# Performance work log

Hardware: AMD Instinct MI355X
Metric: run time of the kernel (lower is better)

The kernel has to match this reference:

```python
import jax, jax.numpy as jnp
import numpy as np

N = 50000
E = 800000
F_IN = 128


def _gat(h, src, dst, W, a_src, a_dst, bias, heads, out_ch, concat):
    n = h.shape[0]
    z = (h @ W.T).reshape(n, heads, out_ch)              # [N,H,C]
    alpha_s = jnp.sum(z * a_src, axis=-1)                # [N,H]
    alpha_d = jnp.sum(z * a_dst, axis=-1)                # [N,H]
    logits = jax.nn.leaky_relu(alpha_s[src] + alpha_d[dst], 0.2)  # [Etot,H]
    m = jax.ops.segment_max(logits, dst, num_segments=n)
    ex = jnp.exp(logits - m[dst])
    denom = jax.ops.segment_sum(ex, dst, num_segments=n)
    w = ex / (denom[dst] + 1e-16)                        # [Etot,H]
    agg = jax.ops.segment_sum(w[:, :, None] * z[src], dst, num_segments=n)  # [N,H,C]
    if concat:
        out = agg.reshape(n, heads * out_ch)
    else:
        out = agg.mean(axis=1)
    return out + bias


def setup_inputs() -> dict:
    key = jax.random.key(0)
    ks = jax.random.split(key, 16)
    s = lambda *sh: 1.0 / np.sqrt(sh[-1])
    inp = {
        "x": jax.random.normal(ks[0], (N, F_IN), jnp.float32),
        "edge_index": jax.random.randint(ks[1], (2, E), 0, N, jnp.int64),
        # GraphConv(no_node_features=128 -> 128, aggr='add')
        "W_rel": jax.random.normal(ks[2], (128, F_IN), jnp.float32) * s(128, F_IN),
        "b_rel": jnp.zeros((128,), jnp.float32),
        "W_root": jax.random.normal(ks[3], (128, F_IN), jnp.float32) * s(128, F_IN),
        # GATConv(128 -> 8, heads=8, concat) => 64
        "W1": jax.random.normal(ks[4], (64, 128), jnp.float32) * s(64, 128),
        "a1_src": jax.random.normal(ks[5], (8, 8), jnp.float32) * 0.35,
        "a1_dst": jax.random.normal(ks[6], (8, 8), jnp.float32) * 0.35,
        "b1": jnp.zeros((64,), jnp.float32),
        # GATConv(64 -> 64, heads=1, concat=False)
        "W2": jax.random.normal(ks[7], (64, 64), jnp.float32) * s(64, 64),
        "a2_src": jax.random.normal(ks[8], (1, 64), jnp.float32) * 0.125,
        "a2_dst": jax.random.normal(ks[9], (1, 64), jnp.float32) * 0.125,
        "b2": jnp.zeros((64,), jnp.float32),
        "Wr": jax.random.normal(ks[10], (1, 64), jnp.float32) * s(1, 64),
        "br": jnp.zeros((1,), jnp.float32),
    }
    return inp


def reference(x, edge_index, W_rel, b_rel, W_root, W1, a1_src, a1_dst, b1,
              W2, a2_src, a2_dst, b2, Wr, br):
    src, dst = edge_index[0], edge_index[1]
    # GraphConv, aggr='add': W_rel @ sum_{j in N(i)} x_j + b + W_root @ x_i
    nbr = jax.ops.segment_sum(x[src], dst, num_segments=N)
    h = nbr @ W_rel.T + b_rel + x @ W_root.T
    h = jax.nn.elu(h)
    # GATConv adds self-loops by default
    loop = jnp.arange(N, dtype=edge_index.dtype)
    src2 = jnp.concatenate([src, loop])
    dst2 = jnp.concatenate([dst, loop])
    h = _gat(h, src2, dst2, W1, a1_src, a1_dst, b1, heads=8, out_ch=8, concat=True)
    h = jax.nn.elu(h)
    h = _gat(h, src2, dst2, W2, a2_src, a2_dst, b2, heads=1, out_ch=64, concat=False)
    # final 'mean' aggregation over all nodes (single graph)
    g = jnp.mean(h, axis=0, keepdims=True)               # [1,64]
    return g @ Wr.T + br                                  # [1,1]
```

## Files before the change

### kernel.cpp

```cpp
#include <hip/hip_runtime.h>
#include <hip/hip_bf16.h>
#include <math.h>

#define N_NODES 50000
#define N_EDGES 800000
#define F_IN 128
#define NBUCK 391
#define EPB 4096
#define NBB 196

typedef __attribute__((ext_vector_type(8))) short bf16x8;
typedef __attribute__((ext_vector_type(4))) float f32x4;
typedef __attribute__((ext_vector_type(2))) float f32x2;
typedef unsigned long long ull;

__device__ __forceinline__ float elu_f(float x)   { return x > 0.f ? x : expm1f(x); }
__device__ __forceinline__ float lrelu_f(float x) { return x > 0.f ? x : 0.2f * x; }
__device__ __forceinline__ int   clampN(int v)    { return v < 0 ? 0 : (v >= N_NODES ? N_NODES - 1 : v); }
__device__ __forceinline__ float bits2f(unsigned int u) { union { unsigned int u; float f; } x; x.u = u; return x.f; }
__device__ __forceinline__ float bf2f(unsigned short s) { return bits2f(((unsigned int)s) << 16); }
__device__ __forceinline__ unsigned short f2bfbits(float f) {
    __hip_bfloat16 b = __float2bfloat16(f);
    return __builtin_bit_cast(unsigned short, b);
}
__device__ __forceinline__ unsigned int pack2(float lo, float hi) {
    return ((unsigned int)f2bfbits(hi) << 16) | f2bfbits(lo);
}

#define CAST_X_IDS (N_NODES * 32)
#define CAST_IDS (CAST_X_IDS + 32768 + 8192 + 4096)
#define CASTB ((CAST_IDS + 255) / 256)
__global__ __launch_bounds__(256) void k_prep(const int* __restrict__ dst,
                                              const float* __restrict__ x,
                                              const float* __restrict__ W_rel,
                                              const float* __restrict__ W_root,
                                              const float* __restrict__ W1,
                                              const float* __restrict__ W2,
                                              int* __restrict__ part,
                                              __hip_bfloat16* __restrict__ Abuf,
                                              unsigned int* __restrict__ x8,
                                              __hip_bfloat16* __restrict__ Wc,
                                              __hip_bfloat16* __restrict__ W1b,
                                              __hip_bfloat16* __restrict__ W2b,
                                              float* __restrict__ red) {
    __shared__ int hist[NBUCK];
    int tid = threadIdx.x;
    if (blockIdx.x < NBB) {
        for (int j = tid; j < NBUCK; j += 256) hist[j] = 0;
        __syncthreads();
        int base = blockIdx.x * EPB;
        #pragma unroll
        for (int t = 0; t < EPB / 256; ++t) {
            int e = base + t * 256 + tid;
            if (e < N_EDGES) atomicAdd(&hist[clampN(dst[e]) >> 7], 1);
        }
        __syncthreads();
        for (int j = tid; j < NBUCK; j += 256)
            part[(size_t)blockIdx.x * NBUCK + j] = hist[j];
    } else {
        if (blockIdx.x == NBB) red[tid] = 0.f;
        int id = (blockIdx.x - NBB) * 256 + tid;
        if (id < CAST_X_IDS) {
            int i = id >> 5, c4 = (id & 31) * 4;
            float4 v = *(const float4*)&x[(size_t)i * 128 + c4];
            ull p = (ull)f2bfbits(v.x) | ((ull)f2bfbits(v.y) << 16)
                  | ((ull)f2bfbits(v.z) << 32) | ((ull)f2bfbits(v.w) << 48);
            *(ull*)&Abuf[(size_t)i * 256 + 128 + c4] = p;
            int t = __builtin_amdgcn_cvt_pk_fp8_f32(v.x, v.y, 0, false);
            t = __builtin_amdgcn_cvt_pk_fp8_f32(v.z, v.w, t, true);
            x8[(size_t)i * 32 + (id & 31)] = (unsigned int)t;
        } else if (id < CAST_IDS) {
            int j = id - CAST_X_IDS;
            if (j < 32768) {
                int cc = j >> 8, k = j & 255;
                float v = (k < 128) ? W_rel[cc * 128 + k] : W_root[cc * 128 + (k - 128)];
                Wc[j] = __float2bfloat16(v);
            } else if (j < 32768 + 8192) {
                W1b[j - 32768] = __float2bfloat16(W1[j - 32768]);
            } else {
                W2b[j - 32768 - 8192] = __float2bfloat16(W2[j - 32768 - 8192]);
            }
        }
    }
}

__global__ __launch_bounds__(512) void k_bscan(const int* __restrict__ part,
                                               int* __restrict__ boff,
                                               int* __restrict__ bcur) {
    __shared__ int wsum[8];
    __shared__ int wbase[8];
    int tid = threadIdx.x;
    int lane = tid & 63, wid = tid >> 6;
    int v = 0;
    if (tid < NBUCK) {
        for (int b = 0; b < NBB; ++b) v += part[(size_t)b * NBUCK + tid];
    }
    int x = v;
    #pragma unroll
    for (int d = 1; d < 64; d <<= 1) {
        int t = __shfl_up(x, d, 64);
        if (lane >= d) x += t;
    }
    if (lane == 63) wsum[wid] = x;
    __syncthreads();
    if (tid == 0) {
        int b = 0;
        #pragma unroll
        for (int w = 0; w < 8; ++w) { wbase[w] = b; b += wsum[w]; }
    }
    __syncthreads();
    if (tid < NBUCK) {
        int e = wbase[wid] + x - v;
        boff[tid] = e;
        bcur[tid] = e;
    }
    if (tid == 0) boff[NBUCK] = N_EDGES;
}

__global__ __launch_bounds__(256) void k_bscatter(const int* __restrict__ src,
                                                  const int* __restrict__ dst,
                                                  int* __restrict__ bcur,
                                                  unsigned int* __restrict__ ebuf) {
    __shared__ int hist[NBUCK];
    __shared__ int hbase[NBUCK];
    int tid = threadIdx.x;
    for (int j = tid; j < NBUCK; j += 256) hist[j] = 0;
    __syncthreads();
    int base = blockIdx.x * EPB;
    unsigned int myP[EPB / 256]; int myB[EPB / 256], myR[EPB / 256];
    #pragma unroll
    for (int t = 0; t < EPB / 256; ++t) {
        int e = base + t * 256 + tid;
        if (e < N_EDGES) {
            int d = clampN(dst[e]);
            int s = clampN(src[e]);
            myP[t] = ((unsigned int)s << 7) | (unsigned int)(d & 127);
            myB[t] = d >> 7;
            myR[t] = atomicAdd(&hist[d >> 7], 1);
        } else myB[t] = -1;
    }
    __syncthreads();
    for (int j = tid; j < NBUCK; j += 256)
        if (hist[j]) hbase[j] = atomicAdd(&bcur[j], hist[j]);
    __syncthreads();
    #pragma unroll
    for (int t = 0; t < EPB / 256; ++t) {
        if (myB[t] >= 0) ebuf[hbase[myB[t]] + myR[t]] = myP[t];
    }
}

__global__ __launch_bounds__(256) void k_bfinal(const unsigned int* __restrict__ ebuf,
                                                const int* __restrict__ boff,
                                                int* __restrict__ offsets,
                                                int* __restrict__ csr) {
    __shared__ int cnt[128];
    __shared__ int cur[128];
    __shared__ int ws[4];
    int b = blockIdx.x;
    int tid = threadIdx.x;
    int node0 = b << 7;
    int k0 = boff[b], k1 = boff[b + 1];
    if (tid < 128) cnt[tid] = 0;
    __syncthreads();
    for (int k = k0 + tid; k < k1; k += 256)
        atomicAdd(&cnt[ebuf[k] & 127u], 1);
    __syncthreads();
    int lane = tid & 63;
    int v = (tid < 128) ? cnt[tid] : 0;
    int x = v;
    #pragma unroll
    for (int d = 1; d < 64; d <<= 1) {
        int t = __shfl_up(x, d, 64);
        if (lane >= d) x += t;
    }
    if (lane == 63) ws[tid >> 6] = x;
    __syncthreads();
    if (tid < 128) {
        int add = (tid >> 6) ? ws[0] : 0;
        int excl = k0 + add + x - v;
        cur[tid] = excl;
        int node = node0 + tid;
        if (node < N_NODES) offsets[node] = excl;
    }
    if (b == NBUCK - 1 && tid == 0) offsets[N_NODES] = N_EDGES;
    __syncthreads();
    for (int k = k0 + tid; k < k1; k += 256) {
        unsigned int e = ebuf[k];
        int r = atomicAdd(&cur[e & 127u], 1);
        csr[r] = (int)(e >> 7);
    }
}

__global__ __launch_bounds__(256) void k_gather(const unsigned int* __restrict__ x8,
                                                const int* __restrict__ offsets,
                                                const int* __restrict__ csr,
                                                ull* __restrict__ outNbr) {
    int i = blockIdx.x * 8 + (threadIdx.x >> 5);
    int l = threadIdx.x & 31;
    int k0 = offsets[i], k1 = offsets[i + 1];
    float a0 = 0.f, a1 = 0.f, a2 = 0.f, a3 = 0.f;
    for (int kb = k0; kb < k1; kb += 8) {
        int s[8]; int vm[8];
        #pragma unroll
        for (int j = 0; j < 8; ++j) {
            int kk = kb + j;
            vm[j] = kk < k1;
            s[j] = csr[vm[j] ? kk : k1 - 1];
        }
        unsigned int u[8];
        #pragma unroll
        for (int j = 0; j < 8; ++j) u[j] = x8[(size_t)s[j] * 32 + l];
        #pragma unroll
        for (int j = 0; j < 8; ++j) {
            if (vm[j]) {
                f32x2 lo = __builtin_amdgcn_cvt_pk_f32_fp8(u[j], false);
                f32x2 hi = __builtin_amdgcn_cvt_pk_f32_fp8(u[j], true);
                a0 += lo.x; a1 += lo.y; a2 += hi.x; a3 += hi.y;
            }
        }
    }
    outNbr[(size_t)i * 64 + l] = (ull)pack2(a0, a1) | ((ull)pack2(a2, a3) << 32);
}

__global__ __launch_bounds__(256) void k_gemm12(const __hip_bfloat16* __restrict__ A,
                                                const __hip_bfloat16* __restrict__ Wc,
                                                const float* __restrict__ bias,
                                                const __hip_bfloat16* __restrict__ W1b,
                                                const float* __restrict__ a_src,
                                                const float* __restrict__ a_dst,
                                                float* __restrict__ as_o,
                                                float* __restrict__ ad_o,
                                                unsigned int* __restrict__ z8) {
    __shared__ __align__(16) short smem[64 * 136];
    short (*sA)[40] = (short(*)[40])smem;
    short (*sW)[40] = (short(*)[40])(smem + 64 * 40);
    int tid = threadIdx.x;
    int lane = tid & 63, wave = tid >> 6;
    int quad = lane >> 4, l16 = lane & 15;
    int node0 = blockIdx.x * 64;
    int srow = tid >> 2, schk = (tid & 3) * 8;
    int ga = node0 + srow; if (ga >= N_NODES) ga = N_NODES - 1;
    const short* Ap = (const short*)A + (size_t)ga * 256 + schk;
    const short* Wp = (const short*)Wc;
    f32x4 acc[8];
    #pragma unroll
    for (int t = 0; t < 8; ++t) acc[t] = (f32x4){0.f, 0.f, 0.f, 0.f};
    for (int k0 = 0; k0 < 256; k0 += 32) {
        *(bf16x8*)&sA[srow][schk] = *(const bf16x8*)(Ap + k0);
        #pragma unroll
        for (int it = 0; it < 2; ++it) {
            int wrow = srow + it * 64;
            *(bf16x8*)&sW[wrow][schk] = *(const bf16x8*)(Wp + (size_t)wrow * 256 + k0 + schk);
        }
        __syncthreads();
        bf16x8 a = *(const bf16x8*)&sA[wave * 16 + l16][quad * 8];
        #pragma unroll
        for (int nt = 0; nt < 8; ++nt) {
            bf16x8 b = *(const bf16x8*)&sW[nt * 16 + l16][quad * 8];
            acc[nt] = __builtin_amdgcn_mfma_f32_16x16x32_bf16(a, b, acc[nt], 0, 0, 0);
        }
        __syncthreads();
    }
    #pragma unroll
    for (int nt = 0; nt < 8; ++nt) {
        int col = nt * 16 + l16;
        float bv = bias[col];
        #pragma unroll
        for (int r = 0; r < 4; ++r) {
            int row = wave * 16 + quad * 4 + r;
            smem[row * 136 + col] = (short)f2bfbits(elu_f(acc[nt][r] + bv));
        }
    }
    __syncthreads();
    f32x4 acc2[4];
    #pragma unroll
    for (int t = 0; t < 4; ++t) acc2[t] = (f32x4){0.f, 0.f, 0.f, 0.f};
    const short* W1p = (const short*)W1b;
    #pragma unroll
    for (int k0 = 0; k0 < 128; k0 += 32) {
        bf16x8 a = *(const bf16x8*)&smem[(wave * 16 + l16) * 136 + k0 + quad * 8];
        #pragma unroll
        for (int nt = 0; nt < 4; ++nt) {
            bf16x8 b = *(const bf16x8*)(W1p + (size_t)(nt * 16 + l16) * 128 + k0 + quad * 8);
            acc2[nt] = __builtin_amdgcn_mfma_f32_16x16x32_bf16(a, b, acc2[nt], 0, 0, 0);
        }
    }
    __syncthreads();
    #pragma unroll
    for (int nt = 0; nt < 4; ++nt) {
        int col = nt * 16 + l16;
        #pragma unroll
        for (int r = 0; r < 4; ++r) {
            int row = wave * 16 + quad * 4 + r;
            smem[row * 72 + col] = (short)f2bfbits(acc2[nt][r]);
        }
    }
    __syncthreads();
    int row = tid >> 2, chunk = tid & 3;
    int gi = node0 + row;
    float v[16];
    bf16x8 c0 = *(const bf16x8*)&smem[row * 72 + chunk * 16];
    bf16x8 c1 = *(const bf16x8*)&smem[row * 72 + chunk * 16 + 8];
    #pragma unroll
    for (int j = 0; j < 8; ++j) {
        v[j]     = bf2f((unsigned short)c0[j]);
        v[8 + j] = bf2f((unsigned short)c1[j]);
    }
    float ps0 = 0.f, pd0 = 0.f, ps1 = 0.f, pd1 = 0.f;
    #pragma unroll
    for (int j = 0; j < 8; ++j) {
        ps0 += v[j] * a_src[chunk * 16 + j];
        pd0 += v[j] * a_dst[chunk * 16 + j];
        ps1 += v[8 + j] * a_src[chunk * 16 + 8 + j];
        pd1 += v[8 + j] * a_dst[chunk * 16 + 8 + j];
    }
    if (gi < N_NODES) {
        as_o[(size_t)gi * 8 + 2 * chunk]     = ps0;
        as_o[(size_t)gi * 8 + 2 * chunk + 1] = ps1;
        ad_o[(size_t)gi * 8 + 2 * chunk]     = pd0;
        ad_o[(size_t)gi * 8 + 2 * chunk + 1] = pd1;
        #pragma unroll
        for (int wi = 0; wi < 4; ++wi) {
            int t = __builtin_amdgcn_cvt_pk_fp8_f32(v[4 * wi], v[4 * wi + 1], 0, false);
            t = __builtin_amdgcn_cvt_pk_fp8_f32(v[4 * wi + 2], v[4 * wi + 3], t, true);
            z8[(size_t)gi * 16 + chunk * 4 + wi] = (unsigned int)t;
        }
    }
}

__global__ __launch_bounds__(256) void k_gat1z2(const unsigned int* __restrict__ z8,
                                                const float* __restrict__ as1,
                                                const float* __restrict__ ad1,
                                                const float* __restrict__ b1,
                                                const int* __restrict__ offsets,
                                                const int* __restrict__ csr,
                                                const __hip_bfloat16* __restrict__ W2b,
                                                const float* __restrict__ a2s,
                                                const float* __restrict__ a2d,
                                                float* __restrict__ as2,
                                                float* __restrict__ ad2,
                                                unsigned int* __restrict__ z2e8) {
    __shared__ __align__(16) short sH2[16 * 72];
    __shared__ __align__(16) short sZ2[16 * 72];
    int iloc = threadIdx.x >> 4;
    int i = blockIdx.x * 16 + iloc;
    int l = threadIdx.x & 15;
    int hd = l >> 1;
    int wh = l & 7, slot = l >> 3;
    int k0 = offsets[i], k1 = offsets[i + 1];
    float ad_h = ad1[(size_t)i * 8 + hd];
    float adw  = ad1[(size_t)i * 8 + wh];
    float e_self = __expf(lrelu_f(as1[(size_t)i * 8 + hd] + ad_h));
    unsigned int uz = z8[(size_t)i * 16 + l];
    f32x2 zlo = __builtin_amdgcn_cvt_pk_f32_fp8(uz, false);
    f32x2 zhi = __builtin_amdgcn_cvt_pk_f32_fp8(uz, true);
    float acc0 = e_self * zlo.x, acc1 = e_self * zlo.y;
    float acc2 = e_self * zhi.x, acc3 = e_self * zhi.y;
    float denp = 0.f;
    for (int kb = k0; kb < k1; kb += 8) {
        int sr[4]; float er[4];
        #pragma unroll
        for (int m = 0; m < 4; ++m) {
            int kk = kb + 2 * m + slot;
            bool v = kk < k1;
            int s = csr[v ? kk : k1 - 1];
            sr[m] = s;
            er[m] = v ? __expf(lrelu_f(as1[(size_t)s * 8 + wh] + adw)) : 0.f;
            denp += er[m];
        }
        int sj[8]; float ej[8]; unsigned int u[8];
        #pragma unroll
        for (int m = 0; m < 4; ++m) {
            #pragma unroll
            for (int sb = 0; sb < 2; ++sb) {
                sj[2 * m + sb] = __shfl(sr[m], sb * 8 + hd, 16);
                ej[2 * m + sb] = __shfl(er[m], sb * 8 + hd, 16);
            }
        }
        #pragma unroll
        for (int j = 0; j < 8; ++j) u[j] = z8[(size_t)sj[j] * 16 + l];
        #pragma unroll
        for (int j = 0; j < 8; ++j) {
            f32x2 alo = __builtin_amdgcn_cvt_pk_f32_fp8(u[j], false);
            f32x2 ahi = __builtin_amdgcn_cvt_pk_f32_fp8(u[j], true);
            acc0 += ej[j] * alo.x; acc1 += ej[j] * alo.y;
            acc2 += ej[j] * ahi.x; acc3 += ej[j] * ahi.y;
        }
    }
    denp += __shfl_xor(denp, 8, 16);
    float den = __shfl(denp, hd, 16) + e_self;
    float inv = 1.f / den;
    float r0 = elu_f(acc0 * inv + b1[4 * l + 0]);
    float r1 = elu_f(acc1 * inv + b1[4 * l + 1]);
    float r2 = elu_f(acc2 * inv + b1[4 * l + 2]);
    float r3 = elu_f(acc3 * inv + b1[4 * l + 3]);
    *(ull*)&sH2[iloc * 72 + 4 * l] = (ull)pack2(r0, r1) | ((ull)pack2(r2, r3) << 32);
    __syncthreads();
    int lane = threadIdx.x & 63, wave = threadIdx.x >> 6;
    int quad = lane >> 4, l16 = lane & 15;
    f32x4 accz = (f32x4){0.f, 0.f, 0.f, 0.f};
    const short* W2p = (const short*)W2b;
    #pragma unroll
    for (int kk0 = 0; kk0 < 64; kk0 += 32) {
        bf16x8 a = *(const bf16x8*)&sH2[l16 * 72 + kk0 + quad * 8];
        bf16x8 b = *(const bf16x8*)(W2p + (size_t)(wave * 16 + l16) * 64 + kk0 + quad * 8);
        accz = __builtin_amdgcn_mfma_f32_16x16x32_bf16(a, b, accz, 0, 0, 0);
    }
    #pragma unroll
    for (int r = 0; r < 4; ++r)
        sZ2[(quad * 4 + r) * 72 + wave * 16 + l16] = (short)f2bfbits(accz[r]);
    __syncthreads();
    ull pz = *(const ull*)&sZ2[iloc * 72 + 4 * l];
    float v0 = bf2f((unsigned short)(pz & 0xffff));
    float v1 = bf2f((unsigned short)((pz >> 16) & 0xffff));
    float v2 = bf2f((unsigned short)((pz >> 32) & 0xffff));
    float v3 = bf2f((unsigned short)(pz >> 48));
    float ps = v0 * a2s[4 * l + 0] + v1 * a2s[4 * l + 1] + v2 * a2s[4 * l + 2] + v3 * a2s[4 * l + 3];
    float pd = v0 * a2d[4 * l + 0] + v1 * a2d[4 * l + 1] + v2 * a2d[4 * l + 2] + v3 * a2d[4 * l + 3];
    #pragma unroll
    for (int d = 8; d >= 1; d >>= 1) {
        ps += __shfl_xor(ps, d, 16);
        pd += __shfl_xor(pd, d, 16);
    }
    if (l == 0) { as2[i] = ps; ad2[i] = pd; }
    int t = __builtin_amdgcn_cvt_pk_fp8_f32(v0, v1, 0, false);
    t = __builtin_amdgcn_cvt_pk_fp8_f32(v2, v3, t, true);
    z2e8[(size_t)i * 16 + l] = (unsigned int)t;
}

__global__ __launch_bounds__(256) void k_gat2attn(const unsigned int* __restrict__ z8,
                                                  const float* __restrict__ as2,
                                                  const float* __restrict__ ad2,
                                                  const float* __restrict__ b2,
                                                  const int* __restrict__ offsets,
                                                  const int* __restrict__ csr,
                                                  const float* __restrict__ Wr,
                                                  float* __restrict__ red) {
    int i = blockIdx.x * 16 + (threadIdx.x >> 4);
    int l = threadIdx.x & 15;
    int k0 = offsets[i], k1 = offsets[i + 1];
    float ad = ad2[i];
    float e_self = __expf(lrelu_f(as2[i] + ad));
    unsigned int uz = z8[(size_t)i * 16 + l];
    f32x2 zlo = __builtin_amdgcn_cvt_pk_f32_fp8(uz, false);
    f32x2 zhi = __builtin_amdgcn_cvt_pk_f32_fp8(uz, true);
    float acc0 = e_self * zlo.x, acc1 = e_self * zlo.y;
    float acc2 = e_self * zhi.x, acc3 = e_self * zhi.y;
    float denp = (l == 0) ? e_self : 0.f;
    for (int kb = k0; kb < k1; kb += 16) {
        int kk = kb + l;
        bool v = kk < k1;
        int s = csr[v ? kk : k1 - 1];
        float e = v ? __expf(lrelu_f(as2[s] + ad)) : 0.f;
        denp += e;
        int nv = k1 - kb; if (nv > 16) nv = 16;
        for (int j0 = 0; j0 < nv; j0 += 8) {
            int sj[8]; float ej[8]; unsigned int u[8];
            #pragma unroll
            for (int j = 0; j < 8; ++j) {
                int idx = (j0 + j) & 15;
                sj[j] = __shfl(s, idx, 16);
                ej[j] = __shfl(e, idx, 16);
            }
            #pragma unroll
            for (int j = 0; j < 8; ++j) u[j] = z8[(size_t)sj[j] * 16 + l];
            #pragma unroll
            for (int j = 0; j < 8; ++j) {
                f32x2 alo = __builtin_amdgcn_cvt_pk_f32_fp8(u[j], false);
                f32x2 ahi = __builtin_amdgcn_cvt_pk_f32_fp8(u[j], true);
                acc0 += ej[j] * alo.x; acc1 += ej[j] * alo.y;
                acc2 += ej[j] * ahi.x; acc3 += ej[j] * ahi.y;
            }
        }
    }
    #pragma unroll
    for (int d = 8; d >= 1; d >>= 1) denp += __shfl_xor(denp, d, 16);
    float inv = 1.f / denp;
    float c = (acc0 * inv + b2[4 * l + 0]) * Wr[4 * l + 0]
            + (acc1 * inv + b2[4 * l + 1]) * Wr[4 * l + 1]
            + (acc2 * inv + b2[4 * l + 2]) * Wr[4 * l + 2]
            + (acc3 * inv + b2[4 * l + 3]) * Wr[4 * l + 3];
    #pragma unroll
    for (int d = 8; d >= 1; d >>= 1) c += __shfl_xor(c, d, 64);
    if (l == 0) atomicAdd(&red[blockIdx.x & 255], c);
}

__global__ void k_finalize(const float* __restrict__ red, const float* __restrict__ br,
                           float* __restrict__ out) {
    int t = threadIdx.x;
    float s = red[t] + red[t + 64] + red[t + 128] + red[t + 192];
    #pragma unroll
    for (int d = 32; d >= 1; d >>= 1) s += __shfl_xor(s, d, 64);
    if (t == 0) out[0] = s * (1.0f / N_NODES) + br[0];
}

extern "C" void kernel_launch(void* const* d_in, const int* in_sizes, int n_in,
                              void* d_out, int out_size, void* d_ws, size_t ws_size,
                              hipStream_t stream) {
    const float* x      = (const float*)d_in[0];
    const int*   edges  = (const int*)d_in[1];
    const float* W_rel  = (const float*)d_in[2];
    const float* b_rel  = (const float*)d_in[3];
    const float* W_root = (const float*)d_in[4];
    const float* W1     = (const float*)d_in[5];
    const float* a1s    = (const float*)d_in[6];
    const float* a1d    = (const float*)d_in[7];
    const float* b1     = (const float*)d_in[8];
    const float* W2     = (const float*)d_in[9];
    const float* a2s    = (const float*)d_in[10];
    const float* a2d    = (const float*)d_in[11];
    const float* b2     = (const float*)d_in[12];
    const float* Wr     = (const float*)d_in[13];
    const float* br     = (const float*)d_in[14];
    float* out = (float*)d_out;

    const int* src = edges;
    const int* dst = edges + N_EDGES;

    char* ws = (char*)d_ws;
    size_t p = 0;
    auto alloc = [&](size_t bytes) -> void* {
        void* r = ws + p;
        p = (p + bytes + 255) & ~(size_t)255;
        return r;
    };
    int*   part    = (int*)alloc((size_t)NBB * NBUCK * 4);
    int*   boff    = (int*)alloc((size_t)(NBUCK + 1) * 4);
    int*   bcur    = (int*)alloc((size_t)NBUCK * 4);
    unsigned int* ebuf = (unsigned int*)alloc((size_t)N_EDGES * 4);
    int*   offsets = (int*)alloc((size_t)(N_NODES + 1) * 4);
    int*   csr     = (int*)alloc((size_t)N_EDGES * 4);
    __hip_bfloat16* Abuf = (__hip_bfloat16*)alloc((size_t)N_NODES * 256 * 2);
    unsigned int* x8 = (unsigned int*)alloc((size_t)N_NODES * 32 * 4);
    __hip_bfloat16* Wc   = (__hip_bfloat16*)alloc((size_t)128 * 256 * 2);
    __hip_bfloat16* W1b  = (__hip_bfloat16*)alloc((size_t)64 * 128 * 2);
    __hip_bfloat16* W2b  = (__hip_bfloat16*)alloc((size_t)64 * 64 * 2);
    float* as1 = (float*)alloc((size_t)N_NODES * 8 * 4);
    float* ad1 = (float*)alloc((size_t)N_NODES * 8 * 4);
    float* as2 = (float*)alloc((size_t)N_NODES * 4);
    float* ad2 = (float*)alloc((size_t)N_NODES * 4);
    unsigned int* z1e8 = (unsigned int*)alloc((size_t)N_NODES * 16 * 4);
    unsigned int* z2e8 = (unsigned int*)alloc((size_t)N_NODES * 16 * 4);
    float* red = (float*)alloc(256 * 4);

    const int MB   = (N_NODES + 63) / 64;
    const int NB8  = N_NODES / 8;
    const int NB16 = N_NODES / 16;

    k_prep    <<<NBB + CASTB, 256, 0, stream>>>(dst, x, W_rel, W_root, W1, W2,
                                                part, Abuf, x8, Wc, W1b, W2b, red);
    k_bscan   <<<1, 512, 0, stream>>>(part, boff, bcur);
    k_bscatter<<<NBB, 256, 0, stream>>>(src, dst, bcur, ebuf);
    k_bfinal  <<<NBUCK, 256, 0, stream>>>(ebuf, boff, offsets, csr);
    k_gather  <<<NB8, 256, 0, stream>>>(x8, offsets, csr, (ull*)Abuf);
    k_gemm12  <<<MB, 256, 0, stream>>>(Abuf, Wc, b_rel, W1b, a1s, a1d, as1, ad1, z1e8);
    k_gat1z2  <<<NB16, 256, 0, stream>>>(z1e8, as1, ad1, b1, offsets, csr,
                                         W2b, a2s, a2d, as2, ad2, z2e8);
    k_gat2attn<<<NB16, 256, 0, stream>>>(z2e8, as2, ad2, b2, offsets, csr, Wr, red);
    k_finalize<<<1, 64, 0, stream>>>(red, br, out);
}
```

Before: 241.6 us.

## Sort nodes by degree into a permutation to balance per-wave work in gather kernels

Builds a degree histogram while the CSR is finalized, then adds a k_perm kernel that counting-sorts node ids into degree bins. The gather and both GAT kernels then process nodes in permuted order, so the lanes of a wave handle nodes with similar edge counts and less time is lost to divergent loop trip counts. The cost is an extra kernel launch, the histogram atomics, and an indirection that scatters node-level loads and stores (offsets, as/ad, outputs) away from sequential order. Degrees are capped into the last bin.

```diff
diff --git a/kernel.cpp b/kernel.cpp
--- a/kernel.cpp
+++ b/kernel.cpp
@@ -8,6 +8,7 @@
 #define NBUCK 391
 #define EPB 4096
 #define NBB 196
+#define NDEGB 64
 
 typedef __attribute__((ext_vector_type(8))) short bf16x8;
 typedef __attribute__((ext_vector_type(4))) float f32x4;
@@ -86,10 +87,14 @@
 
 __global__ __launch_bounds__(512) void k_bscan(const int* __restrict__ part,
                                                int* __restrict__ boff,
-                                               int* __restrict__ bcur) {
+                                               int* __restrict__ bcur,
+                                               int* __restrict__ degHist,
+                                               int* __restrict__ gcur) {
     __shared__ int wsum[8];
     __shared__ int wbase[8];
     int tid = threadIdx.x;
+    if (tid < NDEGB) gcur[tid] = 0;
+    if (tid >= NDEGB && tid < 2 * NDEGB) degHist[tid - NDEGB] = 0;
     int lane = tid & 63, wid = tid >> 6;
     int v = 0;
     if (tid < NBUCK) {
@@ -152,19 +157,29 @@
 __global__ __launch_bounds__(256) void k_bfinal(const unsigned int* __restrict__ ebuf,
                                                 const int* __restrict__ boff,
                                                 int* __restrict__ offsets,
-                                                int* __restrict__ csr) {
+                                                int* __restrict__ csr,
+                                                int* __restrict__ degHist) {
     __shared__ int cnt[128];
     __shared__ int cur[128];
     __shared__ int ws[4];
+    __shared__ int dh[NDEGB];
     int b = blockIdx.x;
     int tid = threadIdx.x;
     int node0 = b << 7;
     int k0 = boff[b], k1 = boff[b + 1];
     if (tid < 128) cnt[tid] = 0;
+    if (tid >= 128 && tid < 128 + NDEGB) dh[tid - 128] = 0;
     __syncthreads();
     for (int k = k0 + tid; k < k1; k += 256)
         atomicAdd(&cnt[ebuf[k] & 127u], 1);
     __syncthreads();
+    if (tid < 128) {
+        int node = node0 + tid;
+        if (node < N_NODES) {
+            int dgb = cnt[tid] > (NDEGB - 1) ? (NDEGB - 1) : cnt[tid];
+            atomicAdd(&dh[dgb], 1);
+        }
+    }
     int lane = tid & 63;
     int v = (tid < 128) ? cnt[tid] : 0;
     int x = v;
@@ -184,6 +199,7 @@
     }
     if (b == NBUCK - 1 && tid == 0) offsets[N_NODES] = N_EDGES;
     __syncthreads();
+    if (tid < NDEGB && dh[tid]) atomicAdd(&degHist[tid], dh[tid]);
     for (int k = k0 + tid; k < k1; k += 256) {
         unsigned int e = ebuf[k];
         int r = atomicAdd(&cur[e & 127u], 1);
@@ -191,11 +207,45 @@
     }
 }
 
+__global__ __launch_bounds__(256) void k_perm(const int* __restrict__ offsets,
+                                              const int* __restrict__ degHist,
+                                              int* __restrict__ gcur,
+                                              int* __restrict__ perm) {
+    __shared__ int base[NDEGB];
+    __shared__ int lh[NDEGB];
+    __shared__ int lbase[NDEGB];
+    int tid = threadIdx.x;
+    if (tid < NDEGB) {
+        int v = degHist[tid];
+        int x = v;
+        #pragma unroll
+        for (int d = 1; d < NDEGB; d <<= 1) {
+            int t = __shfl_up(x, d, 64);
+            if (tid >= d) x += t;
+        }
+        base[tid] = x - v;
+        lh[tid] = 0;
+    }
+    __syncthreads();
+    int i = blockIdx.x * 256 + tid;
+    int bin = 0, rank = 0;
+    if (i < N_NODES) {
+        int deg = offsets[i + 1] - offsets[i];
+        bin = deg > (NDEGB - 1) ? (NDEGB - 1) : deg;
+        rank = atomicAdd(&lh[bin], 1);
+    }
+    __syncthreads();
+    if (tid < NDEGB && lh[tid]) lbase[tid] = atomicAdd(&gcur[tid], lh[tid]);
+    __syncthreads();
+    if (i < N_NODES) perm[base[bin] + lbase[bin] + rank] = i;
+}
+
 __global__ __launch_bounds__(256) void k_gather(const unsigned int* __restrict__ x8,
                                                 const int* __restrict__ offsets,
                                                 const int* __restrict__ csr,
+                                                const int* __restrict__ perm,
                                                 ull* __restrict__ outNbr) {
-    int i = blockIdx.x * 8 + (threadIdx.x >> 5);
+    int i = perm[blockIdx.x * 8 + (threadIdx.x >> 5)];
     int l = threadIdx.x & 31;
     int k0 = offsets[i], k1 = offsets[i + 1];
     float a0 = 0.f, a1 = 0.f, a2 = 0.f, a3 = 0.f;
@@ -334,6 +384,7 @@
                                                 const float* __restrict__ b1,
                                                 const int* __restrict__ offsets,
                                                 const int* __restrict__ csr,
+                                                const int* __restrict__ perm,
                                                 const __hip_bfloat16* __restrict__ W2b,
                                                 const float* __restrict__ a2s,
                                                 const float* __restrict__ a2d,
@@ -343,7 +394,7 @@
     __shared__ __align__(16) short sH2[16 * 72];
     __shared__ __align__(16) short sZ2[16 * 72];
     int iloc = threadIdx.x >> 4;
-    int i = blockIdx.x * 16 + iloc;
+    int i = perm[blockIdx.x * 16 + iloc];
     int l = threadIdx.x & 15;
     int hd = l >> 1;
     int wh = l & 7, slot = l >> 3;
@@ -434,9 +485,10 @@
                                                   const float* __restrict__ b2,
                                                   const int* __restrict__ offsets,
                                                   const int* __restrict__ csr,
+                                                  const int* __restrict__ perm,
                                                   const float* __restrict__ Wr,
                                                   float* __restrict__ red) {
-    int i = blockIdx.x * 16 + (threadIdx.x >> 4);
+    int i = perm[blockIdx.x * 16 + (threadIdx.x >> 4)];
     int l = threadIdx.x & 15;
     int k0 = offsets[i], k1 = offsets[i + 1];
     float ad = ad2[i];
@@ -530,6 +582,9 @@
     unsigned int* ebuf = (unsigned int*)alloc((size_t)N_EDGES * 4);
     int*   offsets = (int*)alloc((size_t)(N_NODES + 1) * 4);
     int*   csr     = (int*)alloc((size_t)N_EDGES * 4);
+    int*   degHist = (int*)alloc((size_t)NDEGB * 4);
+    int*   gcur    = (int*)alloc((size_t)NDEGB * 4);
+    int*   perm    = (int*)alloc((size_t)N_NODES * 4);
     __hip_bfloat16* Abuf = (__hip_bfloat16*)alloc((size_t)N_NODES * 256 * 2);
     unsigned int* x8 = (unsigned int*)alloc((size_t)N_NODES * 32 * 4);
     __hip_bfloat16* Wc   = (__hip_bfloat16*)alloc((size_t)128 * 256 * 2);
@@ -546,16 +601,18 @@
     const int MB   = (N_NODES + 63) / 64;
     const int NB8  = N_NODES / 8;
     const int NB16 = N_NODES / 16;
+    const int PB   = (N_NODES + 255) / 256;
 
     k_prep    <<<NBB + CASTB, 256, 0, stream>>>(dst, x, W_rel, W_root, W1, W2,
                                                 part, Abuf, x8, Wc, W1b, W2b, red);
-    k_bscan   <<<1, 512, 0, stream>>>(part, boff, bcur);
+    k_bscan   <<<1, 512, 0, stream>>>(part, boff, bcur, degHist, gcur);
     k_bscatter<<<NBB, 256, 0, stream>>>(src, dst, bcur, ebuf);
-    k_bfinal  <<<NBUCK, 256, 0, stream>>>(ebuf, boff, offsets, csr);
-    k_gather  <<<NB8, 256, 0, stream>>>(x8, offsets, csr, (ull*)Abuf);
+    k_bfinal  <<<NBUCK, 256, 0, stream>>>(ebuf, boff, offsets, csr, degHist);
+    k_perm    <<<PB, 256, 0, stream>>>(offsets, degHist, gcur, perm);
+    k_gather  <<<NB8, 256, 0, stream>>>(x8, offsets, csr, perm, (ull*)Abuf);
     k_gemm12  <<<MB, 256, 0, stream>>>(Abuf, Wc, b_rel, W1b, a1s, a1d, as1, ad1, z1e8);
-    k_gat1z2  <<<NB16, 256, 0, stream>>>(z1e8, as1, ad1, b1, offsets, csr,
+    k_gat1z2  <<<NB16, 256, 0, stream>>>(z1e8, as1, ad1, b1, offsets, csr, perm,
                                          W2b, a2s, a2d, as2, ad2, z2e8);
-    k_gat2attn<<<NB16, 256, 0, stream>>>(z2e8, as2, ad2, b2, offsets, csr, Wr, red);
+    k_gat2attn<<<NB16, 256, 0, stream>>>(z2e8, as2, ad2, b2, offsets, csr, perm, Wr, red);
     k_finalize<<<1, 64, 0, stream>>>(red, br, out);
 }
```

Result: no change. 244.8 us (+1.3%).
